# Kernel tuning notes

Measured on AMD Instinct MI355X. Metric: run time of the kernel, lower is better.

The kernel has to match this reference:

```python
import jax, jax.numpy as jnp
import numpy as np

N_NODES = 100000
N_EDGES = 600000
D = 128
H = 256


def setup_inputs() -> dict:
    key = jax.random.key(0)
    ks = jax.random.split(key, 8)
    nodes = jax.random.normal(ks[0], (N_NODES, D), dtype=jnp.float32)
    senders = jax.random.randint(ks[1], (N_EDGES,), 0, N_NODES)
    receivers = jax.random.randint(ks[2], (N_EDGES,), 0, N_NODES)
    s = 0.05
    return {
        "nodes": nodes,
        "senders": senders,
        "receivers": receivers,
        "Wm1": jax.random.normal(ks[3], (D, H), dtype=jnp.float32) * s,
        "bm1": jnp.zeros((H,), dtype=jnp.float32),
        "Wm2": jax.random.normal(ks[4], (H, D), dtype=jnp.float32) * s,
        "bm2": jnp.zeros((D,), dtype=jnp.float32),
        "Wn1": jax.random.normal(ks[5], (2 * D, H), dtype=jnp.float32) * s,
        "bn1": jnp.zeros((H,), dtype=jnp.float32),
        "Wn2": jax.random.normal(ks[6], (H, D), dtype=jnp.float32) * s,
        "bn2": jnp.zeros((D,), dtype=jnp.float32),
    }


def reference(nodes, senders, receivers, Wm1, bm1, Wm2, bm2, Wn1, bn1, Wn2, bn2):
    # message MLP applied per node (vmap(message_fn) over nodes)
    m = jax.nn.relu(nodes @ Wm1 + bm1) @ Wm2 + bm2            # [N, D]
    # gather messages along edges by sender, segment_sum to receivers
    agg = jax.ops.segment_sum(m[senders], receivers, num_segments=nodes.shape[0])  # [N, D]
    # node update MLP on [nodes || aggregated messages]
    h = jnp.concatenate([nodes, agg], axis=-1)                # [N, 2D]
    upd = jax.nn.relu(h @ Wn1 + bn1) @ Wn2 + bn2              # [N, D]
    # residual add
    return nodes + upd
```

## Files before the change

kernel.cpp:

```cpp
#include <hip/hip_runtime.h>

#define NN 100000
#define DD 128
#define HH 256
#define NE 600000
#define CAP 32

typedef short bf8 __attribute__((ext_vector_type(8)));
typedef float f32x4 __attribute__((ext_vector_type(4)));
typedef unsigned short u16x8 __attribute__((ext_vector_type(8)));

__device__ __forceinline__ unsigned short f2bf(float f) {
  unsigned int u = __builtin_bit_cast(unsigned int, f);
  u += 0x7fffu + ((u >> 16) & 1u);
  return (unsigned short)(u >> 16);
}
__device__ __forceinline__ float bf2f(unsigned short h) {
  unsigned int u = ((unsigned int)h) << 16;
  return __builtin_bit_cast(float, u);
}

__global__ __launch_bounds__(256) void pack(
    const float* __restrict__ Wm1, const float* __restrict__ Wm2,
    const float* __restrict__ Wn1, const float* __restrict__ Wn2,
    unsigned short* __restrict__ Pm1, unsigned short* __restrict__ Pm2,
    unsigned short* __restrict__ Pn1, unsigned short* __restrict__ Pn2) {
  int b = blockIdx.x;
  const float* W; unsigned short* P; int K, N, base;
  if (b < 16)      { W = Wm1; P = Pm1; K = 128; N = 256; base = 0;  }
  else if (b < 32) { W = Wm2; P = Pm2; K = 256; N = 128; base = 16; }
  else if (b < 64) { W = Wn1; P = Pn1; K = 256; N = 256; base = 32; }
  else             { W = Wn2; P = Pn2; K = 256; N = 128; base = 64; }
  int idx = (b - base) * 256 + threadIdx.x;
  int KT = K >> 5;
  int lane = idx & 63;
  int t = idx >> 6;
  int kt = t % KT, nt = t / KT;
  int n = nt * 16 + (lane & 15);
  int k0 = kt * 32 + (lane >> 4) * 8;
  unsigned short* dst = P + (size_t)idx * 8;
#pragma unroll
  for (int j = 0; j < 8; ++j) dst[j] = f2bf(W[(size_t)(k0 + j) * N + n]);
}

__global__ __launch_bounds__(512) void msg_mlp(
    const float* __restrict__ nodes,
    const unsigned short* __restrict__ W1p, const float* __restrict__ b1,
    const unsigned short* __restrict__ W2p, const float* __restrict__ b2,
    unsigned short* __restrict__ Mb,
    const int* __restrict__ snd, const int* __restrict__ rcv,
    int* __restrict__ cnt, int* __restrict__ ebuf) {
  __shared__ __align__(16) unsigned short h[64][264];
  const int row0 = blockIdx.x * 64;
  const int tid = threadIdx.x;
  const int lane = tid & 63, wave = tid >> 6;
  const int l15 = lane & 15, l4 = lane >> 4;

  {
    int e = blockIdx.x * 512 + tid;
    if (e < NE) {
      int r = rcv[e];
      int pos = atomicAdd(&cnt[r], 1);
      if (pos < CAP) ebuf[r * CAP + pos] = snd[e];
    }
  }

#pragma unroll
  for (int i = 0; i < 2; ++i) {
    int flat = (i * 512 + tid) * 8;
    int r = flat >> 7, c = flat & 127;
    u16x8 o = (u16x8)0;
    if (row0 + r < NN) {
      const float4 v0 = *(const float4*)(nodes + (size_t)(row0 + r) * DD + c);
      const float4 v1 = *(const float4*)(nodes + (size_t)(row0 + r) * DD + c + 4);
      o[0] = f2bf(v0.x); o[1] = f2bf(v0.y); o[2] = f2bf(v0.z); o[3] = f2bf(v0.w);
      o[4] = f2bf(v1.x); o[5] = f2bf(v1.y); o[6] = f2bf(v1.z); o[7] = f2bf(v1.w);
    }
    *(u16x8*)&h[r][c] = o;
  }
  __syncthreads();

  f32x4 acc[2][4];
#pragma unroll
  for (int mt = 0; mt < 2; ++mt)
#pragma unroll
    for (int nt = 0; nt < 4; ++nt) acc[mt][nt] = (f32x4){0.f, 0.f, 0.f, 0.f};
#pragma unroll
  for (int kt = 0; kt < 4; ++kt) {
    bf8 wfr[2], xfr[4];
#pragma unroll
    for (int mt = 0; mt < 2; ++mt) {
      int Htile = wave * 2 + mt;
      wfr[mt] = *(const bf8*)(W1p + ((size_t)(Htile * 4 + kt) * 64 + lane) * 8);
    }
#pragma unroll
    for (int nt = 0; nt < 4; ++nt)
      xfr[nt] = *(const bf8*)&h[nt * 16 + l15][kt * 32 + l4 * 8];
#pragma unroll
    for (int mt = 0; mt < 2; ++mt)
#pragma unroll
      for (int nt = 0; nt < 4; ++nt)
        acc[mt][nt] = __builtin_amdgcn_mfma_f32_16x16x32_bf16(wfr[mt], xfr[nt], acc[mt][nt], 0, 0, 0);
  }
  __syncthreads();

#pragma unroll
  for (int mt = 0; mt < 2; ++mt) {
    int Hbase = wave * 32 + mt * 16 + l4 * 4;
    float4 bv = *(const float4*)(b1 + Hbase);
#pragma unroll
    for (int nt = 0; nt < 4; ++nt) {
      ushort4 o;
      float v0 = acc[mt][nt][0] + bv.x; o.x = f2bf(v0 > 0.f ? v0 : 0.f);
      float v1 = acc[mt][nt][1] + bv.y; o.y = f2bf(v1 > 0.f ? v1 : 0.f);
      float v2 = acc[mt][nt][2] + bv.z; o.z = f2bf(v2 > 0.f ? v2 : 0.f);
      float v3 = acc[mt][nt][3] + bv.w; o.w = f2bf(v3 > 0.f ? v3 : 0.f);
      *(ushort4*)&h[nt * 16 + l15][Hbase] = o;
    }
  }
  __syncthreads();

  f32x4 acc2[4];
#pragma unroll
  for (int nt = 0; nt < 4; ++nt) acc2[nt] = (f32x4){0.f, 0.f, 0.f, 0.f};
#pragma unroll
  for (int kt = 0; kt < 8; ++kt) {
    bf8 wfr, xfr[4];
    wfr = *(const bf8*)(W2p + ((size_t)(wave * 8 + kt) * 64 + lane) * 8);
#pragma unroll
    for (int nt = 0; nt < 4; ++nt)
      xfr[nt] = *(const bf8*)&h[nt * 16 + l15][kt * 32 + l4 * 8];
#pragma unroll
    for (int nt = 0; nt < 4; ++nt)
      acc2[nt] = __builtin_amdgcn_mfma_f32_16x16x32_bf16(wfr, xfr[nt], acc2[nt], 0, 0, 0);
  }
  {
    int Dbase = wave * 16 + l4 * 4;
    float4 bv = *(const float4*)(b2 + Dbase);
#pragma unroll
    for (int nt = 0; nt < 4; ++nt) {
      int node = row0 + nt * 16 + l15;
      if (node < NN) {
        ushort4 o;
        o.x = f2bf(acc2[nt][0] + bv.x);
        o.y = f2bf(acc2[nt][1] + bv.y);
        o.z = f2bf(acc2[nt][2] + bv.z);
        o.w = f2bf(acc2[nt][3] + bv.w);
        *(ushort4*)(Mb + (size_t)node * DD + Dbase) = o;
      }
    }
  }
}

__global__ __launch_bounds__(512) void node_fused(
    const float* __restrict__ nodes, const unsigned short* __restrict__ Mb,
    const int* __restrict__ ebuf, const int* __restrict__ cnt,
    const unsigned short* __restrict__ W1p, const float* __restrict__ b1,
    const unsigned short* __restrict__ W2p, const float* __restrict__ b2,
    float* __restrict__ out) {
  __shared__ __align__(16) unsigned short h[64][264];
  const int row0 = blockIdx.x * 64;
  const int tid = threadIdx.x;
  const int lane = tid & 63, wave = tid >> 6;
  const int l15 = lane & 15, l4 = lane >> 4;
  const int halfid = lane >> 5, sub = lane & 31;

  int degv[4], basev[4], s_all[4][8];
#pragma unroll
  for (int t = 0; t < 4; ++t) {
    int node = row0 + t * 16 + wave * 2 + halfid;
    basev[t] = node * CAP;
    int d = (node < NN) ? cnt[node] : 0;
    degv[t] = d < CAP ? d : CAP;
  }
#pragma unroll
  for (int t = 0; t < 4; ++t)
#pragma unroll
    for (int u = 0; u < 8; ++u) s_all[t][u] = ebuf[basev[t] + u];

#pragma unroll
  for (int i = 0; i < 2; ++i) {
    int flat = (i * 512 + tid) * 8;
    int r = flat >> 7, c = flat & 127;
    u16x8 o = (u16x8)0;
    if (row0 + r < NN) {
      const float4 v0 = *(const float4*)(nodes + (size_t)(row0 + r) * DD + c);
      const float4 v1 = *(const float4*)(nodes + (size_t)(row0 + r) * DD + c + 4);
      o[0] = f2bf(v0.x); o[1] = f2bf(v0.y); o[2] = f2bf(v0.z); o[3] = f2bf(v0.w);
      o[4] = f2bf(v1.x); o[5] = f2bf(v1.y); o[6] = f2bf(v1.z); o[7] = f2bf(v1.w);
    }
    *(u16x8*)&h[r][c] = o;
  }

#pragma unroll
  for (int t = 0; t < 4; ++t) {
    int ln = t * 16 + wave * 2 + halfid;
    int deg = degv[t];
    float a0 = 0.f, a1 = 0.f, a2 = 0.f, a3 = 0.f;
    {
      ushort4 mv[8];
#pragma unroll
      for (int u = 0; u < 8; ++u) {
        int sl = s_all[t][u];
        sl = ((unsigned)sl >= NN) ? 0 : sl;
        mv[u] = *(const ushort4*)(Mb + (size_t)sl * DD + sub * 4);
      }
#pragma unroll
      for (int u = 0; u < 8; ++u) {
        bool act = u < deg;
        a0 += act ? bf2f(mv[u].x) : 0.f;
        a1 += act ? bf2f(mv[u].y) : 0.f;
        a2 += act ? bf2f(mv[u].z) : 0.f;
        a3 += act ? bf2f(mv[u].w) : 0.f;
      }
    }
    for (int bb = 8; bb < deg; bb += 8) {
      int s[8]; ushort4 mv[8];
#pragma unroll
      for (int u = 0; u < 8; ++u) s[u] = ebuf[basev[t] + bb + u];
#pragma unroll
      for (int u = 0; u < 8; ++u) {
        int sl = s[u];
        sl = ((unsigned)sl >= NN) ? 0 : sl;
        mv[u] = *(const ushort4*)(Mb + (size_t)sl * DD + sub * 4);
      }
#pragma unroll
      for (int u = 0; u < 8; ++u) {
        bool act = (bb + u) < deg;
        a0 += act ? bf2f(mv[u].x) : 0.f;
        a1 += act ? bf2f(mv[u].y) : 0.f;
        a2 += act ? bf2f(mv[u].z) : 0.f;
        a3 += act ? bf2f(mv[u].w) : 0.f;
      }
    }
    ushort4 o;
    o.x = f2bf(a0); o.y = f2bf(a1); o.z = f2bf(a2); o.w = f2bf(a3);
    *(ushort4*)&h[ln][128 + sub * 4] = o;
  }
  __syncthreads();

  f32x4 acc[2][4];
#pragma unroll
  for (int mt = 0; mt < 2; ++mt)
#pragma unroll
    for (int nt = 0; nt < 4; ++nt) acc[mt][nt] = (f32x4){0.f, 0.f, 0.f, 0.f};
#pragma unroll
  for (int kt = 0; kt < 8; ++kt) {
    bf8 wfr[2], xfr[4];
#pragma unroll
    for (int mt = 0; mt < 2; ++mt) {
      int Htile = wave * 2 + mt;
      wfr[mt] = *(const bf8*)(W1p + ((size_t)(Htile * 8 + kt) * 64 + lane) * 8);
    }
#pragma unroll
    for (int nt = 0; nt < 4; ++nt)
      xfr[nt] = *(const bf8*)&h[nt * 16 + l15][kt * 32 + l4 * 8];
#pragma unroll
    for (int mt = 0; mt < 2; ++mt)
#pragma unroll
      for (int nt = 0; nt < 4; ++nt)
        acc[mt][nt] = __builtin_amdgcn_mfma_f32_16x16x32_bf16(wfr[mt], xfr[nt], acc[mt][nt], 0, 0, 0);
  }
  __syncthreads();

#pragma unroll
  for (int mt = 0; mt < 2; ++mt) {
    int Hbase = wave * 32 + mt * 16 + l4 * 4;
    float4 bv = *(const float4*)(b1 + Hbase);
#pragma unroll
    for (int nt = 0; nt < 4; ++nt) {
      ushort4 o;
      float v0 = acc[mt][nt][0] + bv.x; o.x = f2bf(v0 > 0.f ? v0 : 0.f);
      float v1 = acc[mt][nt][1] + bv.y; o.y = f2bf(v1 > 0.f ? v1 : 0.f);
      float v2 = acc[mt][nt][2] + bv.z; o.z = f2bf(v2 > 0.f ? v2 : 0.f);
      float v3 = acc[mt][nt][3] + bv.w; o.w = f2bf(v3 > 0.f ? v3 : 0.f);
      *(ushort4*)&h[nt * 16 + l15][Hbase] = o;
    }
  }
  __syncthreads();

  const int Dbase = wave * 16 + l4 * 4;
  float4 rv[4];
#pragma unroll
  for (int nt = 0; nt < 4; ++nt) {
    int node = row0 + nt * 16 + l15;
    rv[nt] = (node < NN) ? *(const float4*)(nodes + (size_t)node * DD + Dbase)
                         : (float4){0.f, 0.f, 0.f, 0.f};
  }

  f32x4 acc2[4];
#pragma unroll
  for (int nt = 0; nt < 4; ++nt) acc2[nt] = (f32x4){0.f, 0.f, 0.f, 0.f};
#pragma unroll
  for (int kt = 0; kt < 8; ++kt) {
    bf8 wfr, xfr[4];
    wfr = *(const bf8*)(W2p + ((size_t)(wave * 8 + kt) * 64 + lane) * 8);
#pragma unroll
    for (int nt = 0; nt < 4; ++nt)
      xfr[nt] = *(const bf8*)&h[nt * 16 + l15][kt * 32 + l4 * 8];
#pragma unroll
    for (int nt = 0; nt < 4; ++nt)
      acc2[nt] = __builtin_amdgcn_mfma_f32_16x16x32_bf16(wfr, xfr[nt], acc2[nt], 0, 0, 0);
  }
  {
    float4 bv = *(const float4*)(b2 + Dbase);
#pragma unroll
    for (int nt = 0; nt < 4; ++nt) {
      int node = row0 + nt * 16 + l15;
      if (node < NN) {
        float4 o;
        o.x = rv[nt].x + acc2[nt][0] + bv.x;
        o.y = rv[nt].y + acc2[nt][1] + bv.y;
        o.z = rv[nt].z + acc2[nt][2] + bv.z;
        o.w = rv[nt].w + acc2[nt][3] + bv.w;
        *(float4*)(out + (size_t)node * DD + Dbase) = o;
      }
    }
  }
}

extern "C" void kernel_launch(void* const* d_in, const int* in_sizes, int n_in,
                              void* d_out, int out_size, void* d_ws, size_t ws_size,
                              hipStream_t stream) {
  const float* nodes = (const float*)d_in[0];
  const int* senders = (const int*)d_in[1];
  const int* receivers = (const int*)d_in[2];
  const float* Wm1 = (const float*)d_in[3];
  const float* bm1 = (const float*)d_in[4];
  const float* Wm2 = (const float*)d_in[5];
  const float* bm2 = (const float*)d_in[6];
  const float* Wn1 = (const float*)d_in[7];
  const float* bn1 = (const float*)d_in[8];
  const float* Wn2 = (const float*)d_in[9];
  const float* bn2 = (const float*)d_in[10];
  float* out = (float*)d_out;

  char* ws = (char*)d_ws;
  unsigned short* Mb   = (unsigned short*)(ws);
  int* cnt    = (int*)(ws + 25600000);
  int* ebuf   = (int*)(ws + 26000000);
  unsigned short* Wm1p = (unsigned short*)(ws + 38800000);
  unsigned short* Wm2p = (unsigned short*)(ws + 38865536);
  unsigned short* Wn1p = (unsigned short*)(ws + 38931072);
  unsigned short* Wn2p = (unsigned short*)(ws + 39062144);

  hipMemsetAsync(cnt, 0, NN * sizeof(int), stream);
  pack<<<80, 256, 0, stream>>>(Wm1, Wm2, Wn1, Wn2, Wm1p, Wm2p, Wn1p, Wn2p);
  msg_mlp<<<1563, 512, 0, stream>>>(nodes, Wm1p, bm1, Wm2p, bm2, Mb,
                                    senders, receivers, cnt, ebuf);
  node_fused<<<1563, 512, 0, stream>>>(nodes, Mb, ebuf, cnt,
                                       Wn1p, bn1, Wn2p, bn2, out);
}
```

Measured before the change: 229.6 us.

## Overlap neighbor gather with first-half node MLP MFMAs; fold cnt reset into pack

The node kernel now runs the first four K-tiles of the node-update GEMM, which depend only on the node features, while the gathered message loads for the aggregation are in flight. This hides gather latency behind MFMA work. The residual is now read from the bf16 copy in shared memory rather than reloaded as fp32 from global, which lowers residual precision. The separate memset of the degree counters is folded into the pack kernel, removing one launch.

```diff
diff --git a/kernel.cpp b/kernel.cpp
--- a/kernel.cpp
+++ b/kernel.cpp
@@ -24,8 +24,12 @@
     const float* __restrict__ Wm1, const float* __restrict__ Wm2,
     const float* __restrict__ Wn1, const float* __restrict__ Wn2,
     unsigned short* __restrict__ Pm1, unsigned short* __restrict__ Pm2,
-    unsigned short* __restrict__ Pn1, unsigned short* __restrict__ Pn2) {
+    unsigned short* __restrict__ Pn1, unsigned short* __restrict__ Pn2,
+    int* __restrict__ cnt) {
   int b = blockIdx.x;
+  int gid = b * 256 + threadIdx.x;
+  for (int i = gid; i < NN; i += 80 * 256) cnt[i] = 0;
+
   const float* W; unsigned short* P; int K, N, base;
   if (b < 16)      { W = Wm1; P = Pm1; K = 128; N = 256; base = 0;  }
   else if (b < 32) { W = Wm2; P = Pm2; K = 256; N = 128; base = 16; }
@@ -165,18 +169,19 @@
   const int l15 = lane & 15, l4 = lane >> 4;
   const int halfid = lane >> 5, sub = lane & 31;
 
-  int degv[4], basev[4], s_all[4][8];
+  int degv[4], basev[4], s1[4][8];
 #pragma unroll
   for (int t = 0; t < 4; ++t) {
     int node = row0 + t * 16 + wave * 2 + halfid;
-    basev[t] = node * CAP;
+    int nodec = (node < NN) ? node : 0;
+    basev[t] = nodec * CAP;
     int d = (node < NN) ? cnt[node] : 0;
     degv[t] = d < CAP ? d : CAP;
   }
 #pragma unroll
   for (int t = 0; t < 4; ++t)
 #pragma unroll
-    for (int u = 0; u < 8; ++u) s_all[t][u] = ebuf[basev[t] + u];
+    for (int u = 0; u < 8; ++u) s1[t][u] = ebuf[basev[t] + u];
 
 #pragma unroll
   for (int i = 0; i < 2; ++i) {
@@ -191,29 +196,113 @@
     }
     *(u16x8*)&h[r][c] = o;
   }
-
-#pragma unroll
-  for (int t = 0; t < 4; ++t) {
-    int ln = t * 16 + wave * 2 + halfid;
+  __syncthreads();
+
+  f32x4 acc[2][4];
+#pragma unroll
+  for (int mt = 0; mt < 2; ++mt)
+#pragma unroll
+    for (int nt = 0; nt < 4; ++nt) acc[mt][nt] = (f32x4){0.f, 0.f, 0.f, 0.f};
+
+  bf8 wfrA[2][2];
+#pragma unroll
+  for (int kt = 0; kt < 2; ++kt)
+#pragma unroll
+    for (int mt = 0; mt < 2; ++mt)
+      wfrA[kt][mt] = *(const bf8*)(W1p + ((size_t)((wave * 2 + mt) * 8 + kt) * 64 + lane) * 8);
+
+  ushort4 mvA[2][8];
+#pragma unroll
+  for (int t = 0; t < 2; ++t)
+#pragma unroll
+    for (int u = 0; u < 8; ++u) {
+      int sl = s1[t][u];
+      sl = ((unsigned)sl >= NN) ? 0 : sl;
+      mvA[t][u] = *(const ushort4*)(Mb + (size_t)sl * DD + sub * 4);
+    }
+
+  const int Dbase = wave * 16 + l4 * 4;
+  ushort4 resid[4];
+#pragma unroll
+  for (int nt = 0; nt < 4; ++nt)
+    resid[nt] = *(ushort4*)&h[nt * 16 + l15][Dbase];
+
+#pragma unroll
+  for (int kt = 0; kt < 2; ++kt) {
+    bf8 xfr[4];
+#pragma unroll
+    for (int nt = 0; nt < 4; ++nt)
+      xfr[nt] = *(const bf8*)&h[nt * 16 + l15][kt * 32 + l4 * 8];
+#pragma unroll
+    for (int mt = 0; mt < 2; ++mt)
+#pragma unroll
+      for (int nt = 0; nt < 4; ++nt)
+        acc[mt][nt] = __builtin_amdgcn_mfma_f32_16x16x32_bf16(wfrA[kt][mt], xfr[nt], acc[mt][nt], 0, 0, 0);
+  }
+
+  float a[4][4];
+#pragma unroll
+  for (int t = 0; t < 2; ++t) {
     int deg = degv[t];
     float a0 = 0.f, a1 = 0.f, a2 = 0.f, a3 = 0.f;
-    {
-      ushort4 mv[8];
-#pragma unroll
-      for (int u = 0; u < 8; ++u) {
-        int sl = s_all[t][u];
-        sl = ((unsigned)sl >= NN) ? 0 : sl;
-        mv[u] = *(const ushort4*)(Mb + (size_t)sl * DD + sub * 4);
-      }
-#pragma unroll
-      for (int u = 0; u < 8; ++u) {
-        bool act = u < deg;
-        a0 += act ? bf2f(mv[u].x) : 0.f;
-        a1 += act ? bf2f(mv[u].y) : 0.f;
-        a2 += act ? bf2f(mv[u].z) : 0.f;
-        a3 += act ? bf2f(mv[u].w) : 0.f;
-      }
-    }
+#pragma unroll
+    for (int u = 0; u < 8; ++u) {
+      bool act = u < deg;
+      a0 += act ? bf2f(mvA[t][u].x) : 0.f;
+      a1 += act ? bf2f(mvA[t][u].y) : 0.f;
+      a2 += act ? bf2f(mvA[t][u].z) : 0.f;
+      a3 += act ? bf2f(mvA[t][u].w) : 0.f;
+    }
+    a[t][0] = a0; a[t][1] = a1; a[t][2] = a2; a[t][3] = a3;
+  }
+
+  bf8 wfrB[2][2];
+#pragma unroll
+  for (int kt = 0; kt < 2; ++kt)
+#pragma unroll
+    for (int mt = 0; mt < 2; ++mt)
+      wfrB[kt][mt] = *(const bf8*)(W1p + ((size_t)((wave * 2 + mt) * 8 + kt + 2) * 64 + lane) * 8);
+  ushort4 mvB[2][8];
+#pragma unroll
+  for (int t = 0; t < 2; ++t)
+#pragma unroll
+    for (int u = 0; u < 8; ++u) {
+      int sl = s1[t + 2][u];
+      sl = ((unsigned)sl >= NN) ? 0 : sl;
+      mvB[t][u] = *(const ushort4*)(Mb + (size_t)sl * DD + sub * 4);
+    }
+
+#pragma unroll
+  for (int kt = 2; kt < 4; ++kt) {
+    bf8 xfr[4];
+#pragma unroll
+    for (int nt = 0; nt < 4; ++nt)
+      xfr[nt] = *(const bf8*)&h[nt * 16 + l15][kt * 32 + l4 * 8];
+#pragma unroll
+    for (int mt = 0; mt < 2; ++mt)
+#pragma unroll
+      for (int nt = 0; nt < 4; ++nt)
+        acc[mt][nt] = __builtin_amdgcn_mfma_f32_16x16x32_bf16(wfrB[kt - 2][mt], xfr[nt], acc[mt][nt], 0, 0, 0);
+  }
+
+#pragma unroll
+  for (int t = 2; t < 4; ++t) {
+    int deg = degv[t];
+    float a0 = 0.f, a1 = 0.f, a2 = 0.f, a3 = 0.f;
+#pragma unroll
+    for (int u = 0; u < 8; ++u) {
+      bool act = u < deg;
+      a0 += act ? bf2f(mvB[t - 2][u].x) : 0.f;
+      a1 += act ? bf2f(mvB[t - 2][u].y) : 0.f;
+      a2 += act ? bf2f(mvB[t - 2][u].z) : 0.f;
+      a3 += act ? bf2f(mvB[t - 2][u].w) : 0.f;
+    }
+    a[t][0] = a0; a[t][1] = a1; a[t][2] = a2; a[t][3] = a3;
+  }
+
+#pragma unroll
+  for (int t = 0; t < 4; ++t) {
+    int deg = degv[t];
     for (int bb = 8; bb < deg; bb += 8) {
       int s[8]; ushort4 mv[8];
 #pragma unroll
@@ -227,31 +316,30 @@
 #pragma unroll
       for (int u = 0; u < 8; ++u) {
         bool act = (bb + u) < deg;
-        a0 += act ? bf2f(mv[u].x) : 0.f;
-        a1 += act ? bf2f(mv[u].y) : 0.f;
-        a2 += act ? bf2f(mv[u].z) : 0.f;
-        a3 += act ? bf2f(mv[u].w) : 0.f;
+        a[t][0] += act ? bf2f(mv[u].x) : 0.f;
+        a[t][1] += act ? bf2f(mv[u].y) : 0.f;
+        a[t][2] += act ? bf2f(mv[u].z) : 0.f;
+        a[t][3] += act ? bf2f(mv[u].w) : 0.f;
       }
     }
+  }
+
+#pragma unroll
+  for (int t = 0; t < 4; ++t) {
+    int ln = t * 16 + wave * 2 + halfid;
     ushort4 o;
-    o.x = f2bf(a0); o.y = f2bf(a1); o.z = f2bf(a2); o.w = f2bf(a3);
+    o.x = f2bf(a[t][0]); o.y = f2bf(a[t][1]);
+    o.z = f2bf(a[t][2]); o.w = f2bf(a[t][3]);
     *(ushort4*)&h[ln][128 + sub * 4] = o;
   }
   __syncthreads();
 
-  f32x4 acc[2][4];
-#pragma unroll
-  for (int mt = 0; mt < 2; ++mt)
-#pragma unroll
-    for (int nt = 0; nt < 4; ++nt) acc[mt][nt] = (f32x4){0.f, 0.f, 0.f, 0.f};
-#pragma unroll
-  for (int kt = 0; kt < 8; ++kt) {
+#pragma unroll
+  for (int kt = 4; kt < 8; ++kt) {
     bf8 wfr[2], xfr[4];
 #pragma unroll
-    for (int mt = 0; mt < 2; ++mt) {
-      int Htile = wave * 2 + mt;
-      wfr[mt] = *(const bf8*)(W1p + ((size_t)(Htile * 8 + kt) * 64 + lane) * 8);
-    }
+    for (int mt = 0; mt < 2; ++mt)
+      wfr[mt] = *(const bf8*)(W1p + ((size_t)((wave * 2 + mt) * 8 + kt) * 64 + lane) * 8);
 #pragma unroll
     for (int nt = 0; nt < 4; ++nt)
       xfr[nt] = *(const bf8*)&h[nt * 16 + l15][kt * 32 + l4 * 8];
@@ -279,15 +367,6 @@
   }
   __syncthreads();
 
-  const int Dbase = wave * 16 + l4 * 4;
-  float4 rv[4];
-#pragma unroll
-  for (int nt = 0; nt < 4; ++nt) {
-    int node = row0 + nt * 16 + l15;
-    rv[nt] = (node < NN) ? *(const float4*)(nodes + (size_t)node * DD + Dbase)
-                         : (float4){0.f, 0.f, 0.f, 0.f};
-  }
-
   f32x4 acc2[4];
 #pragma unroll
   for (int nt = 0; nt < 4; ++nt) acc2[nt] = (f32x4){0.f, 0.f, 0.f, 0.f};
@@ -309,10 +388,10 @@
       int node = row0 + nt * 16 + l15;
       if (node < NN) {
         float4 o;
-        o.x = rv[nt].x + acc2[nt][0] + bv.x;
-        o.y = rv[nt].y + acc2[nt][1] + bv.y;
-        o.z = rv[nt].z + acc2[nt][2] + bv.z;
-        o.w = rv[nt].w + acc2[nt][3] + bv.w;
+        o.x = bf2f(resid[nt].x) + acc2[nt][0] + bv.x;
+        o.y = bf2f(resid[nt].y) + acc2[nt][1] + bv.y;
+        o.z = bf2f(resid[nt].z) + acc2[nt][2] + bv.z;
+        o.w = bf2f(resid[nt].w) + acc2[nt][3] + bv.w;
         *(float4*)(out + (size_t)node * DD + Dbase) = o;
       }
     }
@@ -344,8 +423,7 @@
   unsigned short* Wn1p = (unsigned short*)(ws + 38931072);
   unsigned short* Wn2p = (unsigned short*)(ws + 39062144);
 
-  hipMemsetAsync(cnt, 0, NN * sizeof(int), stream);
-  pack<<<80, 256, 0, stream>>>(Wm1, Wm2, Wn1, Wn2, Wm1p, Wm2p, Wn1p, Wn2p);
+  pack<<<80, 256, 0, stream>>>(Wm1, Wm2, Wn1, Wn2, Wm1p, Wm2p, Wn1p, Wn2p, cnt);
   msg_mlp<<<1563, 512, 0, stream>>>(nodes, Wm1p, bm1, Wm2p, bm2, Mb,
                                     senders, receivers, cnt, ebuf);
   node_fused<<<1563, 512, 0, stream>>>(nodes, Mb, ebuf, cnt,
```

New measurement: 246.3 us. 7.3% more time.

## Cache bf16 node copy for node kernel, fold cnt memset into pack

Applied to the files above, without the earlier changes.

msg_mlp now writes a bf16 copy of the node features to a workspace buffer. node_fused reads that buffer instead of re-reading and converting fp32 nodes, and takes the residual from shared memory rather than a second global fp32 load. The cnt zeroing moves from a hipMemsetAsync into the pack kernel, which removes one launch. In exchange msg_mlp does an extra 25.6 MB write, and the residual add is now done in bf16 precision, which loosens accuracy.

```diff
diff --git a/kernel.cpp b/kernel.cpp
--- a/kernel.cpp
+++ b/kernel.cpp
@@ -24,8 +24,12 @@
     const float* __restrict__ Wm1, const float* __restrict__ Wm2,
     const float* __restrict__ Wn1, const float* __restrict__ Wn2,
     unsigned short* __restrict__ Pm1, unsigned short* __restrict__ Pm2,
-    unsigned short* __restrict__ Pn1, unsigned short* __restrict__ Pn2) {
+    unsigned short* __restrict__ Pn1, unsigned short* __restrict__ Pn2,
+    int* __restrict__ cnt) {
   int b = blockIdx.x;
+  int gid = b * 256 + threadIdx.x;
+  for (int i = gid; i < NN; i += 80 * 256) cnt[i] = 0;
+
   const float* W; unsigned short* P; int K, N, base;
   if (b < 16)      { W = Wm1; P = Pm1; K = 128; N = 256; base = 0;  }
   else if (b < 32) { W = Wm2; P = Pm2; K = 256; N = 128; base = 16; }
@@ -47,7 +51,7 @@
     const float* __restrict__ nodes,
     const unsigned short* __restrict__ W1p, const float* __restrict__ b1,
     const unsigned short* __restrict__ W2p, const float* __restrict__ b2,
-    unsigned short* __restrict__ Mb,
+    unsigned short* __restrict__ Mb, unsigned short* __restrict__ Xb,
     const int* __restrict__ snd, const int* __restrict__ rcv,
     int* __restrict__ cnt, int* __restrict__ ebuf) {
   __shared__ __align__(16) unsigned short h[64][264];
@@ -75,6 +79,7 @@
       const float4 v1 = *(const float4*)(nodes + (size_t)(row0 + r) * DD + c + 4);
       o[0] = f2bf(v0.x); o[1] = f2bf(v0.y); o[2] = f2bf(v0.z); o[3] = f2bf(v0.w);
       o[4] = f2bf(v1.x); o[5] = f2bf(v1.y); o[6] = f2bf(v1.z); o[7] = f2bf(v1.w);
+      *(u16x8*)(Xb + (size_t)(row0 + r) * DD + c) = o;
     }
     *(u16x8*)&h[r][c] = o;
   }
@@ -153,7 +158,7 @@
 }
 
 __global__ __launch_bounds__(512) void node_fused(
-    const float* __restrict__ nodes, const unsigned short* __restrict__ Mb,
+    const unsigned short* __restrict__ Xb, const unsigned short* __restrict__ Mb,
     const int* __restrict__ ebuf, const int* __restrict__ cnt,
     const unsigned short* __restrict__ W1p, const float* __restrict__ b1,
     const unsigned short* __restrict__ W2p, const float* __restrict__ b2,
@@ -165,31 +170,27 @@
   const int l15 = lane & 15, l4 = lane >> 4;
   const int halfid = lane >> 5, sub = lane & 31;
 
-  int degv[4], basev[4], s_all[4][8];
+  int degv[4], basev[4], s1[4][8];
 #pragma unroll
   for (int t = 0; t < 4; ++t) {
     int node = row0 + t * 16 + wave * 2 + halfid;
-    basev[t] = node * CAP;
+    int nodec = (node < NN) ? node : 0;
+    basev[t] = nodec * CAP;
     int d = (node < NN) ? cnt[node] : 0;
     degv[t] = d < CAP ? d : CAP;
   }
 #pragma unroll
   for (int t = 0; t < 4; ++t)
 #pragma unroll
-    for (int u = 0; u < 8; ++u) s_all[t][u] = ebuf[basev[t] + u];
+    for (int u = 0; u < 8; ++u) s1[t][u] = ebuf[basev[t] + u];
 
 #pragma unroll
   for (int i = 0; i < 2; ++i) {
     int flat = (i * 512 + tid) * 8;
     int r = flat >> 7, c = flat & 127;
-    u16x8 o = (u16x8)0;
-    if (row0 + r < NN) {
-      const float4 v0 = *(const float4*)(nodes + (size_t)(row0 + r) * DD + c);
-      const float4 v1 = *(const float4*)(nodes + (size_t)(row0 + r) * DD + c + 4);
-      o[0] = f2bf(v0.x); o[1] = f2bf(v0.y); o[2] = f2bf(v0.z); o[3] = f2bf(v0.w);
-      o[4] = f2bf(v1.x); o[5] = f2bf(v1.y); o[6] = f2bf(v1.z); o[7] = f2bf(v1.w);
-    }
-    *(u16x8*)&h[r][c] = o;
+    u16x8 v = (u16x8)0;
+    if (row0 + r < NN) v = *(const u16x8*)(Xb + (size_t)(row0 + r) * DD + c);
+    *(u16x8*)&h[r][c] = v;
   }
 
 #pragma unroll
@@ -201,7 +202,7 @@
       ushort4 mv[8];
 #pragma unroll
       for (int u = 0; u < 8; ++u) {
-        int sl = s_all[t][u];
+        int sl = s1[t][u];
         sl = ((unsigned)sl >= NN) ? 0 : sl;
         mv[u] = *(const ushort4*)(Mb + (size_t)sl * DD + sub * 4);
       }
@@ -238,6 +239,12 @@
     *(ushort4*)&h[ln][128 + sub * 4] = o;
   }
   __syncthreads();
+
+  const int Dbase = wave * 16 + l4 * 4;
+  ushort4 resid[4];
+#pragma unroll
+  for (int nt = 0; nt < 4; ++nt)
+    resid[nt] = *(ushort4*)&h[nt * 16 + l15][Dbase];
 
   f32x4 acc[2][4];
 #pragma unroll
@@ -279,15 +286,6 @@
   }
   __syncthreads();
 
-  const int Dbase = wave * 16 + l4 * 4;
-  float4 rv[4];
-#pragma unroll
-  for (int nt = 0; nt < 4; ++nt) {
-    int node = row0 + nt * 16 + l15;
-    rv[nt] = (node < NN) ? *(const float4*)(nodes + (size_t)node * DD + Dbase)
-                         : (float4){0.f, 0.f, 0.f, 0.f};
-  }
-
   f32x4 acc2[4];
 #pragma unroll
   for (int nt = 0; nt < 4; ++nt) acc2[nt] = (f32x4){0.f, 0.f, 0.f, 0.f};
@@ -309,10 +307,10 @@
       int node = row0 + nt * 16 + l15;
       if (node < NN) {
         float4 o;
-        o.x = rv[nt].x + acc2[nt][0] + bv.x;
-        o.y = rv[nt].y + acc2[nt][1] + bv.y;
-        o.z = rv[nt].z + acc2[nt][2] + bv.z;
-        o.w = rv[nt].w + acc2[nt][3] + bv.w;
+        o.x = bf2f(resid[nt].x) + acc2[nt][0] + bv.x;
+        o.y = bf2f(resid[nt].y) + acc2[nt][1] + bv.y;
+        o.z = bf2f(resid[nt].z) + acc2[nt][2] + bv.z;
+        o.w = bf2f(resid[nt].w) + acc2[nt][3] + bv.w;
         *(float4*)(out + (size_t)node * DD + Dbase) = o;
       }
     }
@@ -337,17 +335,17 @@
 
   char* ws = (char*)d_ws;
   unsigned short* Mb   = (unsigned short*)(ws);
-  int* cnt    = (int*)(ws + 25600000);
-  int* ebuf   = (int*)(ws + 26000000);
-  unsigned short* Wm1p = (unsigned short*)(ws + 38800000);
-  unsigned short* Wm2p = (unsigned short*)(ws + 38865536);
-  unsigned short* Wn1p = (unsigned short*)(ws + 38931072);
-  unsigned short* Wn2p = (unsigned short*)(ws + 39062144);
-
-  hipMemsetAsync(cnt, 0, NN * sizeof(int), stream);
-  pack<<<80, 256, 0, stream>>>(Wm1, Wm2, Wn1, Wn2, Wm1p, Wm2p, Wn1p, Wn2p);
-  msg_mlp<<<1563, 512, 0, stream>>>(nodes, Wm1p, bm1, Wm2p, bm2, Mb,
+  unsigned short* Xb   = (unsigned short*)(ws + 25600000);
+  int* cnt    = (int*)(ws + 51200000);
+  int* ebuf   = (int*)(ws + 51600000);
+  unsigned short* Wm1p = (unsigned short*)(ws + 64400000);
+  unsigned short* Wm2p = (unsigned short*)(ws + 64465536);
+  unsigned short* Wn1p = (unsigned short*)(ws + 64531072);
+  unsigned short* Wn2p = (unsigned short*)(ws + 64662144);
+
+  pack<<<80, 256, 0, stream>>>(Wm1, Wm2, Wn1, Wn2, Wm1p, Wm2p, Wn1p, Wn2p, cnt);
+  msg_mlp<<<1563, 512, 0, stream>>>(nodes, Wm1p, bm1, Wm2p, bm2, Mb, Xb,
                                     senders, receivers, cnt, ebuf);
-  node_fused<<<1563, 512, 0, stream>>>(nodes, Mb, ebuf, cnt,
+  node_fused<<<1563, 512, 0, stream>>>(Xb, Mb, ebuf, cnt,
                                        Wn1p, bn1, Wn2p, bn2, out);
 }
```

Result: no change. 227.4 us (-0.9%).
